# Kernel tuning notes

Hardware: AMD Instinct MI355X
Metric: run time of the kernel (lower is better)

## Reference

```python
import jax, jax.numpy as jnp
import numpy as np

NUM_HEADS = 8
LN_EPS = 1e-5


def _layernorm(x, g, b):
    mu = jnp.mean(x, axis=-1, keepdims=True)
    var = jnp.mean((x - mu) ** 2, axis=-1, keepdims=True)
    return (x - mu) * jax.lax.rsqrt(var + LN_EPS) * g + b


def setup_inputs() -> dict:
    key = jax.random.key(0)
    B, T, N, D = 16, 12, 325, 128
    F = 256
    ks = jax.random.split(key, 16)
    s = 0.02
    return {
        "x": jax.random.normal(ks[0], (B, T, N, D), dtype=jnp.float32),
        "Wq": jax.random.normal(ks[1], (D, D), dtype=jnp.float32) * s,
        "bq": jnp.zeros((D,), jnp.float32),
        "Wk": jax.random.normal(ks[2], (D, D), dtype=jnp.float32) * s,
        "bk": jnp.zeros((D,), jnp.float32),
        "Wv": jax.random.normal(ks[3], (D, D), dtype=jnp.float32) * s,
        "bv": jnp.zeros((D,), jnp.float32),
        "Wo": jax.random.normal(ks[4], (D, D), dtype=jnp.float32) * s,
        "bo": jnp.zeros((D,), jnp.float32),
        "ln1_g": jnp.ones((D,), jnp.float32),
        "ln1_b": jnp.zeros((D,), jnp.float32),
        "W1": jax.random.normal(ks[5], (D, F), dtype=jnp.float32) * s,
        "b1": jnp.zeros((F,), jnp.float32),
        "W2": jax.random.normal(ks[6], (F, D), dtype=jnp.float32) * s,
        "b2": jnp.zeros((D,), jnp.float32),
        "ln2_g": jnp.ones((D,), jnp.float32),
        "ln2_b": jnp.zeros((D,), jnp.float32),
    }


def reference(x, Wq, bq, Wk, bk, Wv, bv, Wo, bo, ln1_g, ln1_b, W1, b1, W2, b2, ln2_g, ln2_b):
    B, T, N, D = x.shape
    H = NUM_HEADS
    hd = D // H
    # Conv2d 1x1 projections == per-channel linear over last dim
    q = (x @ Wq + bq).reshape(B, T, N, H, hd)
    k = (x @ Wk + bk).reshape(B, T, N, H, hd)
    v = (x @ Wv + bv).reshape(B, T, N, H, hd)
    # attention across the node dim (n,m), per (batch, head, time)
    scores = jnp.einsum("btnhd,btmhd->bhtnm", q, k) / jnp.sqrt(jnp.float32(hd))
    attn = jax.nn.softmax(scores, axis=-1)
    out = jnp.einsum("bhtnm,btmhd->btnhd", attn, v).reshape(B, T, N, D)
    out = out @ Wo + bo
    out = _layernorm(x + out, ln1_g, ln1_b)
    ffn = jax.nn.gelu(out @ W1 + b1, approximate=False) @ W2 + b2
    return _layernorm(out + ffn, ln2_g, ln2_b)
```

## Files before the change

kernel.cpp:

```cpp
#include <hip/hip_runtime.h>
#include <hip/hip_bf16.h>
#include <math.h>

#define B_ 16
#define T_ 12
#define N_ 325
#define D_ 128
#define H_ 8
#define HD_ 16
#define F_ 256
#define ROWS (B_*T_*N_)
#define NP 336
#define QK_STRIDE 20
#define VT_STRIDE 340
#define LN_EPS 1e-5f

typedef __hip_bfloat16 bf16;
typedef __attribute__((ext_vector_type(8))) short bf16x8;
typedef __attribute__((ext_vector_type(4))) short bf16x4;
typedef __attribute__((ext_vector_type(4))) float f32x4;

__device__ __forceinline__ float b2f(bf16 v) { return __bfloat162float(v); }
__device__ __forceinline__ bf16  f2b(float v) { return __float2bfloat16(v); }

__device__ __forceinline__ float fexp2(float v) { return __builtin_amdgcn_exp2f(v); }
__device__ __forceinline__ float frcp(float v) { return __builtin_amdgcn_rcpf(v); }

union frag_cvt  { uint4 u; bf16x8 s; };
union frag4_cvt { uint2 u; bf16x4 s; };
union h2u       { __hip_bfloat162 h; unsigned u; };

__device__ __forceinline__ bf16x8 frag_ld(const void* p) {
    frag_cvt c; c.u = *(const uint4*)p; return c.s;
}
__device__ __forceinline__ bf16x4 frag4_ld(const void* p) {
    frag4_cvt c; c.u = *(const uint2*)p; return c.s;
}

__device__ __forceinline__ unsigned pk2(float a, float b) {
    h2u c; c.h = __float22bfloat162_rn(make_float2(a, b)); return c.u;
}

__device__ __forceinline__ bf16x4 pack4_rtn(f32x4 v) {
    frag4_cvt c;
    c.u.x = pk2(v[0], v[1]);
    c.u.y = pk2(v[2], v[3]);
    return c.s;
}

__device__ __forceinline__ bf16x8 pack8_rtn(float4 a, float4 b) {
    frag_cvt c;
    c.u.x = pk2(a.x, a.y);
    c.u.y = pk2(a.z, a.w);
    c.u.z = pk2(b.x, b.y);
    c.u.w = pk2(b.z, b.w);
    return c.s;
}

__device__ __forceinline__ float gelu_fast(float a) {
    float z = fexp2(2.3022083f * a * (1.f + 0.044715f * a * a));
    return a * z * frcp(z + 1.f);
}

#define MFMA16(a_, b_, c_) __builtin_amdgcn_mfma_f32_16x16x16bf16_1k((a_), (b_), (c_), 0, 0, 0)
#define MFMA32(a_, b_, c_) __builtin_amdgcn_mfma_f32_16x16x32_bf16((a_), (b_), (c_), 0, 0, 0)

__global__ void convert_weights(const float* __restrict__ Wq, const float* __restrict__ Wk,
                                const float* __restrict__ Wv, const float* __restrict__ Wo,
                                const float* __restrict__ W1, const float* __restrict__ W2,
                                bf16* __restrict__ wt) {
    int i = blockIdx.x * 256 + threadIdx.x;
    if (i < 16384)       { int k = i >> 7, n = i & 127;                    wt[n * 128 + k] = f2b(Wq[i]); }
    else if (i < 32768)  { int j = i - 16384; int k = j >> 7, n = j & 127; wt[16384 + n * 128 + k] = f2b(Wk[j]); }
    else if (i < 49152)  { int j = i - 32768; int k = j >> 7, n = j & 127; wt[32768 + n * 128 + k] = f2b(Wv[j]); }
    else if (i < 65536)  { int j = i - 49152; int k = j >> 7, n = j & 127;
                           wt[49152 + n * 128 + (k ^ ((n & 7) << 3))] = f2b(Wo[j]); }
    else if (i < 98304)  { int j = i - 65536; int k = j >> 8, n = j & 255;
                           wt[65536 + n * 128 + (k ^ ((n & 7) << 3))] = f2b(W1[j]); }
    else                 { int j = i - 98304; int k = j >> 7, n = j & 127;
                           wt[98304 + n * 256 + (k ^ ((n & 7) << 3))] = f2b(W2[j]); }
}

__global__ __launch_bounds__(256) void qkv_attn_kernel(
        const float* __restrict__ x, const bf16* __restrict__ wt,
        const float* __restrict__ bq, const float* __restrict__ bk,
        const float* __restrict__ bv, bf16* __restrict__ ao) {
    __shared__ __align__(16) bf16 qsh[NP * QK_STRIDE];
    __shared__ __align__(16) bf16 ksh[NP * QK_STRIDE];
    __shared__ __align__(16) bf16 vsh_t[HD_ * VT_STRIDE];

    int bid  = blockIdx.x;
    int bt   = bid % 192;
    int h    = bid / 192;
    int tid  = threadIdx.x;
    int wave = tid >> 6;
    int lane = tid & 63;
    int lm   = lane & 15;
    int quad = lane >> 4;

    bf16x8 bfrag[3][4];
    #pragma unroll
    for (int mat = 0; mat < 3; mat++) {
        const bf16* Wt = wt + mat * 16384 + (size_t)(h * 16 + lm) * 128;
        #pragma unroll
        for (int ks = 0; ks < 4; ks++)
            bfrag[mat][ks] = frag_ld(Wt + ks * 32 + quad * 8);
    }
    float bqv = bq[h * 16 + lm], bkv = bk[h * 16 + lm], bvv = bv[h * 16 + lm];
    const float QSCALE = 0.25f * 1.44269504f;

    const float* xslab = x + (size_t)bt * N_ * D_;
    for (int mt = wave; mt < 21; mt += 4) {
        int row  = mt * 16 + lm;
        int crow = row < N_ ? row : N_ - 1;
        const float* xr = xslab + (size_t)crow * D_;
        bf16x8 af[4];
        #pragma unroll
        for (int ks = 0; ks < 4; ks++) {
            const float4* p = (const float4*)(xr + ks * 32 + quad * 8);
            af[ks] = pack8_rtn(p[0], p[1]);
        }
        f32x4 cq = {0.f,0.f,0.f,0.f}, ck = {0.f,0.f,0.f,0.f}, cv = {0.f,0.f,0.f,0.f};
        #pragma unroll
        for (int ks = 0; ks < 4; ks++) {
            cq = MFMA32(af[ks], bfrag[0][ks], cq);
            ck = MFMA32(af[ks], bfrag[1][ks], ck);
            cv = MFMA32(af[ks], bfrag[2][ks], cv);
        }
        #pragma unroll
        for (int reg = 0; reg < 4; reg++) {
            int r = mt * 16 + quad * 4 + reg;
            bool v = r < N_;
            qsh[r * QK_STRIDE + lm]  = f2b(v ? (cq[reg] + bqv) * QSCALE : 0.f);
            ksh[r * QK_STRIDE + lm]  = f2b(v ? (ck[reg] + bkv) : 0.f);
            vsh_t[lm * VT_STRIDE + r] = f2b(v ? (cv[reg] + bvv) : 0.f);
        }
    }
    __syncthreads();

    const f32x4 zero = {0.f, 0.f, 0.f, 0.f};
    for (int qt0 = wave; qt0 < 21; qt0 += 8) {
        int qt1  = qt0 + 4;
        int qt1c = qt1 < 21 ? qt1 : 20;
        bf16x4 qf0 = frag4_ld(qsh + (qt0  * 16 + lm) * QK_STRIDE + quad * 4);
        bf16x4 qf1 = frag4_ld(qsh + (qt1c * 16 + lm) * QK_STRIDE + quad * 4);
        f32x4 o0 = zero, o1 = zero;
        float L0 = 0.f, L1 = 0.f;
        for (int kt = 0; kt < 20; kt++) {
            bf16x4 kf = frag4_ld(ksh + (kt * 16 + lm) * QK_STRIDE + quad * 4);
            bf16x4 vf = frag4_ld(vsh_t + lm * VT_STRIDE + kt * 16 + quad * 4);
            f32x4 s0 = MFMA16(kf, qf0, zero);
            f32x4 s1 = MFMA16(kf, qf1, zero);
            f32x4 p0, p1;
            p0[0] = fexp2(s0[0]); p0[1] = fexp2(s0[1]);
            p0[2] = fexp2(s0[2]); p0[3] = fexp2(s0[3]);
            p1[0] = fexp2(s1[0]); p1[1] = fexp2(s1[1]);
            p1[2] = fexp2(s1[2]); p1[3] = fexp2(s1[3]);
            L0 += (p0[0] + p0[1]) + (p0[2] + p0[3]);
            L1 += (p1[0] + p1[1]) + (p1[2] + p1[3]);
            o0 = MFMA16(vf, pack4_rtn(p0), o0);
            o1 = MFMA16(vf, pack4_rtn(p1), o1);
        }
        {
            bf16x4 kf = frag4_ld(ksh + (20 * 16 + lm) * QK_STRIDE + quad * 4);
            bf16x4 vf = frag4_ld(vsh_t + lm * VT_STRIDE + 20 * 16 + quad * 4);
            f32x4 s0 = MFMA16(kf, qf0, zero);
            f32x4 s1 = MFMA16(kf, qf1, zero);
            f32x4 p0, p1;
            #pragma unroll
            for (int reg = 0; reg < 4; reg++) {
                bool ok = (quad * 4 + reg) < 5;
                p0[reg] = ok ? fexp2(s0[reg]) : 0.f;
                p1[reg] = ok ? fexp2(s1[reg]) : 0.f;
            }
            L0 += (p0[0] + p0[1]) + (p0[2] + p0[3]);
            L1 += (p1[0] + p1[1]) + (p1[2] + p1[3]);
            o0 = MFMA16(vf, pack4_rtn(p0), o0);
            o1 = MFMA16(vf, pack4_rtn(p1), o1);
        }
        L0 += __shfl_xor(L0, 16, 64); L0 += __shfl_xor(L0, 32, 64);
        L1 += __shfl_xor(L1, 16, 64); L1 += __shfl_xor(L1, 32, 64);
        float i0 = frcp(L0), i1 = frcp(L1);
        int n0 = qt0 * 16 + lm;
        if (n0 < N_) {
            frag4_cvt o;
            o.u.x = pk2(o0[0] * i0, o0[1] * i0);
            o.u.y = pk2(o0[2] * i0, o0[3] * i0);
            *(uint2*)(ao + ((size_t)bt * N_ + n0) * D_ + h * HD_ + quad * 4) = o.u;
        }
        int n1 = qt1 * 16 + lm;
        if (qt1 < 21 && n1 < N_) {
            frag4_cvt o;
            o.u.x = pk2(o1[0] * i1, o1[1] * i1);
            o.u.y = pk2(o1[2] * i1, o1[3] * i1);
            *(uint2*)(ao + ((size_t)bt * N_ + n1) * D_ + h * HD_ + quad * 4) = o.u;
        }
    }
}

#define US_STRIDE 136
#define H_STRIDE  264

__global__ __launch_bounds__(256) void epilogue_mfma(
        const float* __restrict__ x, const bf16* __restrict__ ao,
        const bf16* __restrict__ wt,
        const float* __restrict__ bo,
        const float* __restrict__ g1, const float* __restrict__ be1,
        const float* __restrict__ fb1, const float* __restrict__ fb2,
        const float* __restrict__ g2, const float* __restrict__ be2,
        float* __restrict__ out) {
    __shared__ __align__(16) bf16 wbuf[32768];
    __shared__ __align__(16) bf16 us_lds[4][16 * US_STRIDE];
    __shared__ __align__(16) bf16 h_lds[4][16 * H_STRIDE];

    const bf16* Wot = wt + 49152;
    const bf16* W1t = wt + 65536;
    const bf16* W2t = wt + 98304;

    int tid  = threadIdx.x;
    int wave = tid >> 6;
    int lm   = tid & 15;
    int quad = (tid & 63) >> 4;
    int r0   = blockIdx.x * 64 + wave * 16;
    int sw   = (lm & 7) << 3;

    bf16* us = us_lds[wave];
    bf16* hh = h_lds[wave];

    bf16x8 afrag[8];

    {
        const bf16* ar = ao + (size_t)(r0 + lm) * D_;
        #pragma unroll
        for (int ks = 0; ks < 4; ks++)
            afrag[ks] = frag_ld(ar + ks * 32 + quad * 8);
    }

    {
        const uint4* gs = (const uint4*)Wot;
        uint4*       ls = (uint4*)wbuf;
        #pragma unroll
        for (int i = 0; i < 8; i++) ls[tid + i * 256] = gs[tid + i * 256];
    }
    __syncthreads();

    f32x4 acc[8];
    #pragma unroll
    for (int nt = 0; nt < 8; nt++) {
        f32x4 c = {0.f, 0.f, 0.f, 0.f};
        const bf16* w = wbuf + (size_t)(nt * 16 + lm) * 128;
        #pragma unroll
        for (int ks = 0; ks < 4; ks++) {
            bf16x8 b = frag_ld(w + ((ks * 32 + quad * 8) ^ sw));
            c = MFMA32(afrag[ks], b, c);
        }
        acc[nt] = c;
    }

    float bov[8], g1v[8], be1v[8], g2v[8], be2v[8], fb2v[8];
    #pragma unroll
    for (int nt = 0; nt < 8; nt++) {
        int col = nt * 16 + lm;
        bov[nt] = bo[col]; g1v[nt] = g1[col]; be1v[nt] = be1[col];
        g2v[nt] = g2[col]; be2v[nt] = be2[col]; fb2v[nt] = fb2[col];
    }
    float usv[8][4];
    #pragma unroll
    for (int rg = 0; rg < 4; rg++) {
        int grow = r0 + quad * 4 + rg;
        const float* xr = x + (size_t)grow * D_;
        float rr[8];
        float s = 0.f, s2 = 0.f;
        #pragma unroll
        for (int nt = 0; nt < 8; nt++) {
            rr[nt] = acc[nt][rg] + bov[nt] + xr[nt * 16 + lm];
            s += rr[nt]; s2 += rr[nt] * rr[nt];
        }
        #pragma unroll
        for (int mk = 1; mk < 16; mk <<= 1) {
            s += __shfl_xor(s, mk, 64); s2 += __shfl_xor(s2, mk, 64);
        }
        float mu  = s * (1.f / 128.f);
        float var = s2 * (1.f / 128.f) - mu * mu;
        float rstd = rsqrtf(var + LN_EPS);
        int lrow = quad * 4 + rg;
        #pragma unroll
        for (int nt = 0; nt < 8; nt++) {
            float u = (rr[nt] - mu) * rstd * g1v[nt] + be1v[nt];
            usv[nt][rg] = u;
            us[lrow * US_STRIDE + nt * 16 + lm] = f2b(u);
        }
    }
    __syncthreads();

    {
        const uint4* gs = (const uint4*)W1t;
        uint4*       ls = (uint4*)wbuf;
        #pragma unroll
        for (int i = 0; i < 16; i++) ls[tid + i * 256] = gs[tid + i * 256];
    }
    __syncthreads();

    #pragma unroll
    for (int ks = 0; ks < 4; ks++)
        afrag[ks] = frag_ld(&us[lm * US_STRIDE + ks * 32 + quad * 8]);
    #pragma unroll
    for (int nt = 0; nt < 16; nt++) {
        f32x4 c = {0.f, 0.f, 0.f, 0.f};
        const bf16* w = wbuf + (size_t)(nt * 16 + lm) * 128;
        #pragma unroll
        for (int ks = 0; ks < 4; ks++) {
            bf16x8 b = frag_ld(w + ((ks * 32 + quad * 8) ^ sw));
            c = MFMA32(afrag[ks], b, c);
        }
        int col = nt * 16 + lm;
        float fb = fb1[col];
        #pragma unroll
        for (int rg = 0; rg < 4; rg++) {
            float hg = gelu_fast(c[rg] + fb);
            hh[(quad * 4 + rg) * H_STRIDE + col] = f2b(hg);
        }
    }
    __syncthreads();

    {
        const uint4* gs = (const uint4*)W2t;
        uint4*       ls = (uint4*)wbuf;
        #pragma unroll
        for (int i = 0; i < 16; i++) ls[tid + i * 256] = gs[tid + i * 256];
    }
    __syncthreads();

    #pragma unroll
    for (int ks = 0; ks < 8; ks++)
        afrag[ks] = frag_ld(&hh[lm * H_STRIDE + ks * 32 + quad * 8]);
    #pragma unroll
    for (int nt = 0; nt < 8; nt++) {
        f32x4 c = {0.f, 0.f, 0.f, 0.f};
        const bf16* w = wbuf + (size_t)(nt * 16 + lm) * 256;
        #pragma unroll
        for (int ks = 0; ks < 8; ks++) {
            bf16x8 b = frag_ld(w + ((ks * 32 + quad * 8) ^ sw));
            c = MFMA32(afrag[ks], b, c);
        }
        acc[nt] = c;
    }
    #pragma unroll
    for (int rg = 0; rg < 4; rg++) {
        float yy[8];
        float s = 0.f, s2 = 0.f;
        #pragma unroll
        for (int nt = 0; nt < 8; nt++) {
            yy[nt] = acc[nt][rg] + fb2v[nt] + usv[nt][rg];
            s += yy[nt]; s2 += yy[nt] * yy[nt];
        }
        #pragma unroll
        for (int mk = 1; mk < 16; mk <<= 1) {
            s += __shfl_xor(s, mk, 64); s2 += __shfl_xor(s2, mk, 64);
        }
        float mu  = s * (1.f / 128.f);
        float var = s2 * (1.f / 128.f) - mu * mu;
        float rstd = rsqrtf(var + LN_EPS);
        int grow = r0 + quad * 4 + rg;
        float* orow = out + (size_t)grow * D_;
        #pragma unroll
        for (int nt = 0; nt < 8; nt++)
            orow[nt * 16 + lm] = (yy[nt] - mu) * rstd * g2v[nt] + be2v[nt];
    }
}

extern "C" void kernel_launch(void* const* d_in, const int* in_sizes, int n_in,
                              void* d_out, int out_size, void* d_ws, size_t ws_size,
                              hipStream_t stream) {
    const float* x   = (const float*)d_in[0];
    const float* Wq  = (const float*)d_in[1];
    const float* bq  = (const float*)d_in[2];
    const float* Wk  = (const float*)d_in[3];
    const float* bk  = (const float*)d_in[4];
    const float* Wv  = (const float*)d_in[5];
    const float* bv  = (const float*)d_in[6];
    const float* Wo  = (const float*)d_in[7];
    const float* bo  = (const float*)d_in[8];
    const float* g1  = (const float*)d_in[9];
    const float* be1 = (const float*)d_in[10];
    const float* W1  = (const float*)d_in[11];
    const float* fb1 = (const float*)d_in[12];
    const float* W2  = (const float*)d_in[13];
    const float* fb2 = (const float*)d_in[14];
    const float* g2  = (const float*)d_in[15];
    const float* be2 = (const float*)d_in[16];
    float* out = (float*)d_out;

    bf16* wt = (bf16*)d_ws;
    bf16* ao = wt + 131072;

    convert_weights<<<512, 256, 0, stream>>>(Wq, Wk, Wv, Wo, W1, W2, wt);
    qkv_attn_kernel<<<B_ * T_ * H_, 256, 0, stream>>>(x, wt, bq, bk, bv, ao);
    epilogue_mfma<<<ROWS / 64, 256, 0, stream>>>(x, ao, wt, bo, g1, be1, fb1, fb2,
                                                 g2, be2, out);
}
```

Baseline: 206.0 us.

## Triple-buffer epilogue weight tiles in LDS to overlap loads and drop barriers

Replaces the single 64KB weight buffer with three 32KB LDS buffers. Wo and the first half of W1 are loaded together, then the next weight half-tile is staged into a free buffer while MFMA work runs on the current one. This removes several __syncthreads barriers and lets global-to-LDS copies overlap with compute. Total LDS rises to about 146KB, which raises pressure on the per-CU budget, and each GEMM is now split into two halves.

```diff
diff --git a/kernel.cpp b/kernel.cpp
--- a/kernel.cpp
+++ b/kernel.cpp
@@ -209,7 +209,9 @@
         const float* __restrict__ fb1, const float* __restrict__ fb2,
         const float* __restrict__ g2, const float* __restrict__ be2,
         float* __restrict__ out) {
-    __shared__ __align__(16) bf16 wbuf[32768];
+    __shared__ __align__(16) bf16 bufA[16384];
+    __shared__ __align__(16) bf16 bufB[16384];
+    __shared__ __align__(16) bf16 bufC[16384];
     __shared__ __align__(16) bf16 us_lds[4][16 * US_STRIDE];
     __shared__ __align__(16) bf16 h_lds[4][16 * H_STRIDE];
 
@@ -237,10 +239,14 @@
     }
 
     {
-        const uint4* gs = (const uint4*)Wot;
-        uint4*       ls = (uint4*)wbuf;
-        #pragma unroll
-        for (int i = 0; i < 8; i++) ls[tid + i * 256] = gs[tid + i * 256];
+        const uint4* gs0 = (const uint4*)Wot;
+        const uint4* gs1 = (const uint4*)W1t;
+        uint4* lA = (uint4*)bufA;
+        uint4* lB = (uint4*)bufB;
+        #pragma unroll
+        for (int i = 0; i < 8; i++) lA[tid + i * 256] = gs0[tid + i * 256];
+        #pragma unroll
+        for (int i = 0; i < 8; i++) lB[tid + i * 256] = gs1[tid + i * 256];
     }
     __syncthreads();
 
@@ -248,7 +254,7 @@
     #pragma unroll
     for (int nt = 0; nt < 8; nt++) {
         f32x4 c = {0.f, 0.f, 0.f, 0.f};
-        const bf16* w = wbuf + (size_t)(nt * 16 + lm) * 128;
+        const bf16* w = bufA + (size_t)(nt * 16 + lm) * 128;
         #pragma unroll
         for (int ks = 0; ks < 4; ks++) {
             bf16x8 b = frag_ld(w + ((ks * 32 + quad * 8) ^ sw));
@@ -291,13 +297,11 @@
             us[lrow * US_STRIDE + nt * 16 + lm] = f2b(u);
         }
     }
-    __syncthreads();
-
     {
-        const uint4* gs = (const uint4*)W1t;
-        uint4*       ls = (uint4*)wbuf;
-        #pragma unroll
-        for (int i = 0; i < 16; i++) ls[tid + i * 256] = gs[tid + i * 256];
+        const uint4* gs = ((const uint4*)W1t) + 2048;
+        uint4* lC = (uint4*)bufC;
+        #pragma unroll
+        for (int i = 0; i < 8; i++) lC[tid + i * 256] = gs[tid + i * 256];
     }
     __syncthreads();
 
@@ -305,9 +309,9 @@
     for (int ks = 0; ks < 4; ks++)
         afrag[ks] = frag_ld(&us[lm * US_STRIDE + ks * 32 + quad * 8]);
     #pragma unroll
-    for (int nt = 0; nt < 16; nt++) {
+    for (int nt = 0; nt < 8; nt++) {
         f32x4 c = {0.f, 0.f, 0.f, 0.f};
-        const bf16* w = wbuf + (size_t)(nt * 16 + lm) * 128;
+        const bf16* w = bufB + (size_t)(nt * 16 + lm) * 128;
         #pragma unroll
         for (int ks = 0; ks < 4; ks++) {
             bf16x8 b = frag_ld(w + ((ks * 32 + quad * 8) ^ sw));
@@ -321,13 +325,28 @@
             hh[(quad * 4 + rg) * H_STRIDE + col] = f2b(hg);
         }
     }
-    __syncthreads();
-
+    #pragma unroll
+    for (int nt = 8; nt < 16; nt++) {
+        f32x4 c = {0.f, 0.f, 0.f, 0.f};
+        const bf16* w = bufC + (size_t)((nt - 8) * 16 + lm) * 128;
+        #pragma unroll
+        for (int ks = 0; ks < 4; ks++) {
+            bf16x8 b = frag_ld(w + ((ks * 32 + quad * 8) ^ sw));
+            c = MFMA32(afrag[ks], b, c);
+        }
+        int col = nt * 16 + lm;
+        float fb = fb1[col];
+        #pragma unroll
+        for (int rg = 0; rg < 4; rg++) {
+            float hg = gelu_fast(c[rg] + fb);
+            hh[(quad * 4 + rg) * H_STRIDE + col] = f2b(hg);
+        }
+    }
     {
         const uint4* gs = (const uint4*)W2t;
-        uint4*       ls = (uint4*)wbuf;
-        #pragma unroll
-        for (int i = 0; i < 16; i++) ls[tid + i * 256] = gs[tid + i * 256];
+        uint4* lA = (uint4*)bufA;
+        #pragma unroll
+        for (int i = 0; i < 8; i++) lA[tid + i * 256] = gs[tid + i * 256];
     }
     __syncthreads();
 
@@ -335,9 +354,28 @@
     for (int ks = 0; ks < 8; ks++)
         afrag[ks] = frag_ld(&hh[lm * H_STRIDE + ks * 32 + quad * 8]);
     #pragma unroll
-    for (int nt = 0; nt < 8; nt++) {
+    for (int nt = 0; nt < 4; nt++) {
         f32x4 c = {0.f, 0.f, 0.f, 0.f};
-        const bf16* w = wbuf + (size_t)(nt * 16 + lm) * 256;
+        const bf16* w = bufA + (size_t)(nt * 16 + lm) * 256;
+        #pragma unroll
+        for (int ks = 0; ks < 8; ks++) {
+            bf16x8 b = frag_ld(w + ((ks * 32 + quad * 8) ^ sw));
+            c = MFMA32(afrag[ks], b, c);
+        }
+        acc[nt] = c;
+    }
+    {
+        const uint4* gs = ((const uint4*)W2t) + 2048;
+        uint4* lB = (uint4*)bufB;
+        #pragma unroll
+        for (int i = 0; i < 8; i++) lB[tid + i * 256] = gs[tid + i * 256];
+    }
+    __syncthreads();
+
+    #pragma unroll
+    for (int nt = 4; nt < 8; nt++) {
+        f32x4 c = {0.f, 0.f, 0.f, 0.f};
+        const bf16* w = bufB + (size_t)((nt - 4) * 16 + lm) * 256;
         #pragma unroll
         for (int ks = 0; ks < 8; ks++) {
             bf16x8 b = frag_ld(w + ((ks * 32 + quad * 8) ^ sw));
```

After: 205.9 us. Within noise of the previous version (-0.1%).
